# Performance work log

Measured on AMD Instinct MI355X. Metric: run time of the kernel, lower is better.

The kernel has to match this reference:

```python
import jax, jax.numpy as jnp
import numpy as np

N_NODES = 100000
N_EDGES = 3200000
N_GRAPHS = 256
VOCAB = 1500


def gcn_conv(x, edge_index, W, b, n_nodes):
    # x: [N, Fin], edge_index: [2, E] (row=source, col=target)
    h = x @ W  # [N, Fout]
    loops = jnp.arange(n_nodes, dtype=edge_index.dtype)
    row = jnp.concatenate([edge_index[0], loops])
    col = jnp.concatenate([edge_index[1], loops])
    # symmetric normalization with self-loops (PyG GCNConv default)
    deg = jax.ops.segment_sum(jnp.ones_like(col, dtype=h.dtype), col,
                              num_segments=n_nodes)
    dinv = jnp.where(deg > 0, jax.lax.rsqrt(deg), 0.0)
    norm = dinv[row] * dinv[col]  # [E+N]
    msg = h[row] * norm[:, None]  # gather + scale
    out = jax.ops.segment_sum(msg, col, num_segments=n_nodes)  # scatter-add
    return out + b


def setup_inputs() -> dict:
    key = jax.random.key(0)
    k = jax.random.split(key, 8)
    x_ids = jax.random.randint(k[0], (N_NODES,), 0, VOCAB)
    edge_index = jax.random.randint(k[1], (2, N_EDGES), 0, N_NODES)
    batch = jnp.sort(jax.random.randint(k[2], (N_NODES,), 0, N_GRAPHS))
    emb_table = jax.random.normal(k[3], (VOCAB, 16), dtype=jnp.float32)
    W1 = jax.random.normal(k[4], (16, 32), dtype=jnp.float32) * (1.0 / np.sqrt(16))
    b1 = jnp.zeros((32,), dtype=jnp.float32)
    W2 = jax.random.normal(k[5], (32, 41), dtype=jnp.float32) * (1.0 / np.sqrt(32))
    b2 = jnp.zeros((41,), dtype=jnp.float32)
    return {"x_ids": x_ids, "edge_index": edge_index, "batch": batch,
            "emb_table": emb_table, "W1": W1, "b1": b1, "W2": W2, "b2": b2}


def reference(x_ids, edge_index, batch, emb_table, W1, b1, W2, b2):
    x = emb_table[x_ids]                      # embedding lookup [N,16]
    x = gcn_conv(x, edge_index, W1, b1, N_NODES)
    x = jax.nn.relu(x)                        # dropout is identity in eval
    x = gcn_conv(x, edge_index, W2, b2, N_NODES)
    # scatter_add pooling over graphs in batch
    return jax.ops.segment_sum(x, batch, num_segments=N_GRAPHS)  # [G,41]
```

## Files before the change

### kernel.cpp

```cpp
#include <hip/hip_runtime.h>


constexpr int EPB = 16384;
constexpr int BSH = 8;
constexpr int BKTN = 1 << BSH;
constexpr int CAP = 10240;

__device__ inline unsigned short f2bf(float x) {
  unsigned u = __float_as_uint(x);
  u += 0x7FFF + ((u >> 16) & 1);
  return (unsigned short)(u >> 16);
}
__device__ inline float bf2f(unsigned short h) {
  return __uint_as_float((unsigned)h << 16);
}
__device__ inline unsigned pk(float a, float b) {
  return (unsigned)f2bf(a) | ((unsigned)f2bf(b) << 16);
}

__device__ __forceinline__ int swz(int b, int nblkp) {
  return (b & 7) * (nblkp >> 3) + (b >> 3);
}

__global__ __launch_bounds__(1024) void k_hist(const int* __restrict__ col, int E,
                                               int nbkt, int nblkp,
                                               int* __restrict__ hist) {
  __shared__ int h[512];
  int tid = threadIdx.x;
  int blk = swz(blockIdx.x, nblkp);
  for (int i = tid; i < nbkt; i += 1024) h[i] = 0;
  __syncthreads();
  int e0 = blk * EPB, e1 = min(E, e0 + EPB);
  for (int e = e0 + tid; e < e1; e += 1024) atomicAdd(&h[col[e] >> BSH], 1);
  __syncthreads();
  for (int b = tid; b < nbkt; b += 1024) hist[b * nblkp + blk] = h[b];
}

__global__ __launch_bounds__(1024) void k_scan_a(const int* __restrict__ hist, int tot,
                                                 int* __restrict__ off,
                                                 int* __restrict__ bsums) {
  __shared__ int sd[1024];
  int tid = threadIdx.x;
  int i = blockIdx.x * 1024 + tid;
  int v = (i < tot) ? hist[i] : 0;
  sd[tid] = v;
  __syncthreads();
  for (int o = 1; o < 1024; o <<= 1) {
    int u = (tid >= o) ? sd[tid - o] : 0;
    __syncthreads();
    sd[tid] += u;
    __syncthreads();
  }
  if (i < tot) off[i] = sd[tid] - v;
  if (tid == 1023) bsums[blockIdx.x] = sd[tid];
}

__global__ __launch_bounds__(1024) void k_scan_c(int tot, int nblkp, int nbkt, int E,
                                                 int nscan,
                                                 const int* __restrict__ bsums,
                                                 int* __restrict__ off,
                                                 int* __restrict__ bucket_off) {
  __shared__ int sd[1024];
  int tid = threadIdx.x, b = blockIdx.x;
  sd[tid] = (tid < b && tid < nscan) ? bsums[tid] : 0;
  __syncthreads();
  for (int o = 512; o >= 1; o >>= 1) {
    if (tid < o) sd[tid] += sd[tid + o];
    __syncthreads();
  }
  int sbase = sd[0];
  int i = b * 1024 + tid;
  if (i < tot) {
    int v = off[i] + sbase;
    off[i] = v;
    if (i % nblkp == 0) bucket_off[i / nblkp] = v;
  }
  if (i == 0) bucket_off[nbkt] = E;
}

__global__ __launch_bounds__(1024) void k_scatter(const int* __restrict__ row,
                                                  const int* __restrict__ col, int E,
                                                  int nbkt, int nblkp,
                                                  const int* __restrict__ off,
                                                  int* __restrict__ staging) {
  __shared__ int base[512];
  __shared__ int cur[512];
  int tid = threadIdx.x;
  int blk = swz(blockIdx.x, nblkp);
  for (int b = tid; b < nbkt; b += 1024) {
    base[b] = off[b * nblkp + blk];
    cur[b] = 0;
  }
  __syncthreads();
  int e0 = blk * EPB, e1 = min(E, e0 + EPB);
  for (int e = e0 + tid; e < e1; e += 1024) {
    int c = col[e];
    int b = c >> BSH;
    int rk = atomicAdd(&cur[b], 1);
    staging[base[b] + rk] = (row[e] << BSH) | (c & (BKTN - 1));
  }
}

__global__ __launch_bounds__(BKTN) void k_degprep(const int* __restrict__ staging,
                                                  const int* __restrict__ bucket_off,
                                                  const int* __restrict__ x_ids,
                                                  const float* __restrict__ emb,
                                                  int N,
                                                  float* __restrict__ dinv,
                                                  unsigned short* __restrict__ ag1) {
  __shared__ int cnt[BKTN];
  int tid = threadIdx.x, b = blockIdx.x;
  int beg = bucket_off[b], end = bucket_off[b + 1];
  cnt[tid] = 0;
  __syncthreads();
  for (int i = beg + tid; i < end; i += BKTN)
    atomicAdd(&cnt[staging[i] & (BKTN - 1)], 1);
  __syncthreads();
  int node = (b << BSH) + tid;
  if (node >= N) return;
  float d = rsqrtf((float)(cnt[tid] + 1));
  dinv[node] = d;
  const float* er = emb + (size_t)x_ids[node] * 16;
  float4 e0 = *(const float4*)(er);
  float4 e1 = *(const float4*)(er + 4);
  float4 e2 = *(const float4*)(er + 8);
  float4 e3 = *(const float4*)(er + 12);
  uint4 o0, o1;
  o0.x = pk(e0.x * d, e0.y * d); o0.y = pk(e0.z * d, e0.w * d);
  o0.z = pk(e1.x * d, e1.y * d); o0.w = pk(e1.z * d, e1.w * d);
  o1.x = pk(e2.x * d, e2.y * d); o1.y = pk(e2.z * d, e2.w * d);
  o1.z = pk(e3.x * d, e3.y * d); o1.w = pk(e3.z * d, e3.w * d);
  *(uint4*)(ag1 + (size_t)node * 16) = o0;
  *(uint4*)(ag1 + (size_t)node * 16 + 8) = o1;
}

__global__ __launch_bounds__(512) void k_fuse1(const unsigned short* __restrict__ ag1,
                                               const int* __restrict__ staging,
                                               const int* __restrict__ bucket_off,
                                               const float* __restrict__ dinv,
                                               const float* __restrict__ W1,
                                               const float* __restrict__ b1, int N,
                                               unsigned short* __restrict__ y1g) {
  __shared__ int list[CAP];
  __shared__ int cnt[BKTN], sc[BKTN], lcur[BKTN];
  __shared__ float W[512];
  __shared__ float bb[32];
  int tid = threadIdx.x, b = blockIdx.x;
  W[tid] = W1[tid];
  if (tid < 32) bb[tid] = b1[tid];
  int nloc = tid >> 1, half = tid & 1;
  int node = (b << BSH) + nloc;
  float acc[8];
  if (node < N) {
    uint4 v = *(const uint4*)(ag1 + (size_t)node * 16 + half * 8);
    acc[0] = bf2f(v.x & 0xFFFF); acc[1] = bf2f(v.x >> 16);
    acc[2] = bf2f(v.y & 0xFFFF); acc[3] = bf2f(v.y >> 16);
    acc[4] = bf2f(v.z & 0xFFFF); acc[5] = bf2f(v.z >> 16);
    acc[6] = bf2f(v.w & 0xFFFF); acc[7] = bf2f(v.w >> 16);
  } else {
#pragma unroll
    for (int k = 0; k < 8; ++k) acc[k] = 0.f;
  }
  int beg = bucket_off[b], end = bucket_off[b + 1];
  for (int cbeg = beg; cbeg < end; cbeg += CAP) {
    int cend = min(end, cbeg + CAP);
    if (tid < BKTN) cnt[tid] = 0;
    __syncthreads();
    for (int i = cbeg + tid; i < cend; i += 512)
      atomicAdd(&cnt[staging[i] & (BKTN - 1)], 1);
    __syncthreads();
    if (tid < BKTN) sc[tid] = cnt[tid];
    __syncthreads();
    for (int o = 1; o < BKTN; o <<= 1) {
      int u = (tid < BKTN && tid >= o) ? sc[tid - o] : 0;
      __syncthreads();
      if (tid < BKTN) sc[tid] += u;
      __syncthreads();
    }
    if (tid < BKTN) {
      int st = sc[tid] - cnt[tid];
      sc[tid] = st;
      lcur[tid] = st;
    }
    __syncthreads();
    for (int i = cbeg + tid; i < cend; i += 512) {
      int p = staging[i];
      int pos = atomicAdd(&lcur[p & (BKTN - 1)], 1);
      list[pos] = p >> BSH;
    }
    __syncthreads();
    if (node < N) {
      int st = sc[nloc], dg = cnt[nloc];
      for (int j = 0; j < dg; ++j) {
        int r = list[st + j];
        uint4 v = *(const uint4*)(ag1 + (size_t)r * 16 + half * 8);
        acc[0] += bf2f(v.x & 0xFFFF); acc[1] += bf2f(v.x >> 16);
        acc[2] += bf2f(v.y & 0xFFFF); acc[3] += bf2f(v.y >> 16);
        acc[4] += bf2f(v.z & 0xFFFF); acc[5] += bf2f(v.z >> 16);
        acc[6] += bf2f(v.w & 0xFFFF); acc[7] += bf2f(v.w >> 16);
      }
    }
    __syncthreads();
  }
  if (node >= N) return;
  float d = dinv[node];
  float sx[8], xo[8];
#pragma unroll
  for (int k = 0; k < 8; ++k) sx[k] = acc[k] * d;
#pragma unroll
  for (int k = 0; k < 8; ++k) xo[k] = __shfl_xor(sx[k], 1);
  float x[16];
  if (half == 0) {
#pragma unroll
    for (int k = 0; k < 8; ++k) { x[k] = sx[k]; x[8 + k] = xo[k]; }
  } else {
#pragma unroll
    for (int k = 0; k < 8; ++k) { x[k] = xo[k]; x[8 + k] = sx[k]; }
  }
  int j0 = half * 16;
  float a[16];
#pragma unroll
  for (int j = 0; j < 16; ++j) a[j] = bb[j0 + j];
#pragma unroll
  for (int k = 0; k < 16; ++k) {
    float xv = x[k];
#pragma unroll
    for (int j = 0; j < 16; ++j) a[j] += xv * W[k * 32 + j0 + j];
  }
#pragma unroll
  for (int j = 0; j < 16; ++j) a[j] = fmaxf(a[j], 0.f) * d;
  uint4 o0 = {pk(a[0], a[1]), pk(a[2], a[3]), pk(a[4], a[5]), pk(a[6], a[7])};
  uint4 o1 = {pk(a[8], a[9]), pk(a[10], a[11]), pk(a[12], a[13]), pk(a[14], a[15])};
  unsigned short* yp = y1g + (size_t)half * N * 16 + (size_t)node * 16;
  *(uint4*)(yp) = o0;
  *(uint4*)(yp + 8) = o1;
}

__global__ __launch_bounds__(512) void k_fuse2(const unsigned short* __restrict__ y1p,
                                               const int* __restrict__ staging,
                                               const int* __restrict__ bucket_off,
                                               const float* __restrict__ dinv,
                                               const int* __restrict__ batch, int N,
                                               int pofs, float* __restrict__ P) {
  __shared__ int list[CAP];
  __shared__ int cnt[BKTN], sc[BKTN], lcur[BKTN];
  __shared__ float pool[8 * 16];
  int tid = threadIdx.x, b = blockIdx.x;
  int nloc = tid >> 1, half = tid & 1;
  int node = (b << BSH) + nloc;
  float acc[8];
  if (node < N) {
    uint4 v = *(const uint4*)(y1p + (size_t)node * 16 + half * 8);
    acc[0] = bf2f(v.x & 0xFFFF); acc[1] = bf2f(v.x >> 16);
    acc[2] = bf2f(v.y & 0xFFFF); acc[3] = bf2f(v.y >> 16);
    acc[4] = bf2f(v.z & 0xFFFF); acc[5] = bf2f(v.z >> 16);
    acc[6] = bf2f(v.w & 0xFFFF); acc[7] = bf2f(v.w >> 16);
  } else {
#pragma unroll
    for (int k = 0; k < 8; ++k) acc[k] = 0.f;
  }
  int beg = bucket_off[b], end = bucket_off[b + 1];
  for (int cbeg = beg; cbeg < end; cbeg += CAP) {
    int cend = min(end, cbeg + CAP);
    if (tid < BKTN) cnt[tid] = 0;
    __syncthreads();
    for (int i = cbeg + tid; i < cend; i += 512)
      atomicAdd(&cnt[staging[i] & (BKTN - 1)], 1);
    __syncthreads();
    if (tid < BKTN) sc[tid] = cnt[tid];
    __syncthreads();
    for (int o = 1; o < BKTN; o <<= 1) {
      int u = (tid < BKTN && tid >= o) ? sc[tid - o] : 0;
      __syncthreads();
      if (tid < BKTN) sc[tid] += u;
      __syncthreads();
    }
    if (tid < BKTN) {
      int st = sc[tid] - cnt[tid];
      sc[tid] = st;
      lcur[tid] = st;
    }
    __syncthreads();
    for (int i = cbeg + tid; i < cend; i += 512) {
      int p = staging[i];
      int pos = atomicAdd(&lcur[p & (BKTN - 1)], 1);
      list[pos] = p >> BSH;
    }
    __syncthreads();
    if (node < N) {
      int st = sc[nloc], dg = cnt[nloc];
      for (int j = 0; j < dg; ++j) {
        int r = list[st + j];
        uint4 v = *(const uint4*)(y1p + (size_t)r * 16 + half * 8);
        acc[0] += bf2f(v.x & 0xFFFF); acc[1] += bf2f(v.x >> 16);
        acc[2] += bf2f(v.y & 0xFFFF); acc[3] += bf2f(v.y >> 16);
        acc[4] += bf2f(v.z & 0xFFFF); acc[5] += bf2f(v.z >> 16);
        acc[6] += bf2f(v.w & 0xFFFF); acc[7] += bf2f(v.w >> 16);
      }
    }
    __syncthreads();
  }
  int myg = -1;
  if (node < N) {
    float d = dinv[node];
#pragma unroll
    for (int k = 0; k < 8; ++k) acc[k] *= d;
    myg = batch[node];
  }
  int g0 = batch[b << BSH];
  int g1 = batch[min((b << BSH) + BKTN - 1, N - 1)];
  for (int clo = g0; clo <= g1; clo += 8) {
    for (int j = tid; j < 8 * 16; j += 512) pool[j] = 0.f;
    __syncthreads();
    if (myg >= clo && myg < clo + 8) {
      float* pp = pool + (myg - clo) * 16 + half * 8;
#pragma unroll
      for (int k = 0; k < 8; ++k) atomicAdd(pp + k, acc[k]);
    }
    __syncthreads();
    int ng = min(8, g1 - clo + 1);
    for (int j = tid; j < ng * 16; j += 512)
      atomicAdd(&P[(size_t)(clo + (j >> 4)) * 32 + pofs + (j & 15)], pool[j]);
    __syncthreads();
  }
}

__global__ __launch_bounds__(64) void k_final(const float* __restrict__ P,
                                              const int* __restrict__ batch, int N,
                                              const float* __restrict__ W2,
                                              const float* __restrict__ b2,
                                              float* __restrict__ out) {
  __shared__ float pr[32];
  __shared__ int se[2];
  int g = blockIdx.x, tid = threadIdx.x;
  if (tid < 2) {
    int v = g + tid;
    int lo = 0, hi = N;
    while (lo < hi) {
      int mid = (lo + hi) >> 1;
      if (batch[mid] < v) lo = mid + 1; else hi = mid;
    }
    se[tid] = lo;
  }
  if (tid < 32) pr[tid] = P[(size_t)g * 32 + tid];
  __syncthreads();
  if (tid < 41) {
    float o = (float)(se[1] - se[0]) * b2[tid];
#pragma unroll
    for (int k = 0; k < 32; ++k) o += pr[k] * W2[k * 41 + tid];
    out[(size_t)g * 41 + tid] = o;
  }
}

extern "C" void kernel_launch(void* const* d_in, const int* in_sizes, int n_in,
                              void* d_out, int out_size, void* d_ws, size_t ws_size,
                              hipStream_t stream) {
  const int* x_ids = (const int*)d_in[0];
  const int* edge_index = (const int*)d_in[1];
  const int* batch = (const int*)d_in[2];
  const float* emb = (const float*)d_in[3];
  const float* W1 = (const float*)d_in[4];
  const float* b1 = (const float*)d_in[5];
  const float* W2 = (const float*)d_in[6];
  const float* b2 = (const float*)d_in[7];
  float* out = (float*)d_out;

  const int N = in_sizes[0];
  const int E = in_sizes[1] / 2;
  const int G = out_size / 41;
  const int* row = edge_index;
  const int* col = edge_index + E;

  const int nbkt = (N + BKTN - 1) >> BSH;
  int nblk = (E + EPB - 1) / EPB;
  const int nblkp = (nblk + 7) & ~7;
  const int tot = nbkt * nblkp;
  const int nscan = (tot + 1023) >> 10;

  char* ws = (char*)d_ws;
  size_t woff = 0;
  auto alloc = [&](size_t bytes) -> char* {
    char* p = ws + woff;
    woff += (bytes + 255) & ~(size_t)255;
    return p;
  };
  int* staging = (int*)alloc((size_t)E * 4);
  float* dinv = (float*)alloc((size_t)N * 4);
  unsigned short* ag1 = (unsigned short*)alloc((size_t)N * 16 * 2);
  unsigned short* y1g = (unsigned short*)alloc((size_t)N * 32 * 2);
  int* hist = (int*)alloc((size_t)tot * 4);
  int* off = (int*)alloc((size_t)tot * 4);
  int* bucket_off = (int*)alloc(((size_t)nbkt + 1) * 4);
  int* bsums = (int*)alloc((size_t)nscan * 4);
  float* P = (float*)alloc((size_t)G * 32 * 4);
  (void)ws_size; (void)n_in;

  hipMemsetAsync(P, 0, (size_t)G * 32 * 4, stream);

  k_hist<<<nblkp, 1024, 0, stream>>>(col, E, nbkt, nblkp, hist);
  k_scan_a<<<nscan, 1024, 0, stream>>>(hist, tot, off, bsums);
  k_scan_c<<<nscan, 1024, 0, stream>>>(tot, nblkp, nbkt, E, nscan, bsums, off, bucket_off);
  k_scatter<<<nblkp, 1024, 0, stream>>>(row, col, E, nbkt, nblkp, off, staging);
  k_degprep<<<nbkt, BKTN, 0, stream>>>(staging, bucket_off, x_ids, emb, N, dinv, ag1);
  k_fuse1<<<nbkt, 512, 0, stream>>>(ag1, staging, bucket_off, dinv, W1, b1, N, y1g);
  k_fuse2<<<nbkt, 512, 0, stream>>>(y1g, staging, bucket_off, dinv, batch, N, 0, P);
  k_fuse2<<<nbkt, 512, 0, stream>>>(y1g + (size_t)N * 16, staging, bucket_off, dinv,
                                    batch, N, 16, P);
  k_final<<<G, 64, 0, stream>>>(P, batch, N, W2, b2, out);
}
```

Baseline: 236.6 us.

## Sort edges in LDS before scatter and unroll neighbor gathers by four

The scatter kernel now counts and prefix-sums bucket sizes locally, places each packed edge into a shared-memory buffer grouped by bucket, and then copies each bucket's run to global staging with one wave per bucket. Consecutive lanes now write consecutive global addresses, replacing the scattered per-edge global writes. Both aggregation kernels also unroll the neighbor gather loop four-wide so several independent row loads are in flight at once. The cost is a second read of col, a 64KB LDS buffer that limits occupancy, and extra barriers for the 512-entry scan.

```diff
diff --git a/kernel.cpp b/kernel.cpp
--- a/kernel.cpp
+++ b/kernel.cpp
@@ -16,6 +16,29 @@
 }
 __device__ inline unsigned pk(float a, float b) {
   return (unsigned)f2bf(a) | ((unsigned)f2bf(b) << 16);
+}
+__device__ __forceinline__ void add8(float acc[8], uint4 v) {
+  acc[0] += bf2f(v.x & 0xFFFF); acc[1] += bf2f(v.x >> 16);
+  acc[2] += bf2f(v.y & 0xFFFF); acc[3] += bf2f(v.y >> 16);
+  acc[4] += bf2f(v.z & 0xFFFF); acc[5] += bf2f(v.z >> 16);
+  acc[6] += bf2f(v.w & 0xFFFF); acc[7] += bf2f(v.w >> 16);
+}
+
+__device__ __forceinline__ void gather8(const unsigned short* __restrict__ base,
+                                        const int* list, int st, int dg,
+                                        float acc[8]) {
+  int j = 0;
+  for (; j + 4 <= dg; j += 4) {
+    int r0 = list[st + j], r1 = list[st + j + 1];
+    int r2 = list[st + j + 2], r3 = list[st + j + 3];
+    uint4 v0 = *(const uint4*)(base + (size_t)r0 * 16);
+    uint4 v1 = *(const uint4*)(base + (size_t)r1 * 16);
+    uint4 v2 = *(const uint4*)(base + (size_t)r2 * 16);
+    uint4 v3 = *(const uint4*)(base + (size_t)r3 * 16);
+    add8(acc, v0); add8(acc, v1); add8(acc, v2); add8(acc, v3);
+  }
+  for (; j < dg; ++j)
+    add8(acc, *(const uint4*)(base + (size_t)list[st + j] * 16));
 }
 
 __device__ __forceinline__ int swz(int b, int nblkp) {
@@ -83,21 +106,39 @@
                                                   int nbkt, int nblkp,
                                                   const int* __restrict__ off,
                                                   int* __restrict__ staging) {
-  __shared__ int base[512];
-  __shared__ int cur[512];
+  __shared__ int sbuf[EPB];
+  __shared__ int cnt[512], sc[512], cur[512];
   int tid = threadIdx.x;
+  int lane = tid & 63, wv = tid >> 6;
   int blk = swz(blockIdx.x, nblkp);
-  for (int b = tid; b < nbkt; b += 1024) {
-    base[b] = off[b * nblkp + blk];
-    cur[b] = 0;
-  }
+  if (tid < 512) cnt[tid] = 0;
   __syncthreads();
   int e0 = blk * EPB, e1 = min(E, e0 + EPB);
+  for (int e = e0 + tid; e < e1; e += 1024)
+    atomicAdd(&cnt[col[e] >> BSH], 1);
+  __syncthreads();
+  if (tid < 512) sc[tid] = cnt[tid];
+  __syncthreads();
+  for (int o = 1; o < 512; o <<= 1) {
+    int u = (tid < 512 && tid >= o) ? sc[tid - o] : 0;
+    __syncthreads();
+    if (tid < 512) sc[tid] += u;
+    __syncthreads();
+  }
+  if (tid < 512) { int st = sc[tid] - cnt[tid]; sc[tid] = st; cur[tid] = st; }
+  __syncthreads();
   for (int e = e0 + tid; e < e1; e += 1024) {
     int c = col[e];
     int b = c >> BSH;
-    int rk = atomicAdd(&cur[b], 1);
-    staging[base[b] + rk] = (row[e] << BSH) | (c & (BKTN - 1));
+    int pos = atomicAdd(&cur[b], 1);
+    sbuf[pos] = (row[e] << BSH) | (c & (BKTN - 1));
+  }
+  __syncthreads();
+  for (int b = wv; b < nbkt; b += 16) {
+    int lbeg = sc[b], lcnt = cnt[b];
+    int g = off[b * nblkp + blk];
+    for (int j = lane; j < lcnt; j += 64)
+      staging[g + j] = sbuf[lbeg + j];
   }
 }
 
@@ -189,17 +230,7 @@
       list[pos] = p >> BSH;
     }
     __syncthreads();
-    if (node < N) {
-      int st = sc[nloc], dg = cnt[nloc];
-      for (int j = 0; j < dg; ++j) {
-        int r = list[st + j];
-        uint4 v = *(const uint4*)(ag1 + (size_t)r * 16 + half * 8);
-        acc[0] += bf2f(v.x & 0xFFFF); acc[1] += bf2f(v.x >> 16);
-        acc[2] += bf2f(v.y & 0xFFFF); acc[3] += bf2f(v.y >> 16);
-        acc[4] += bf2f(v.z & 0xFFFF); acc[5] += bf2f(v.z >> 16);
-        acc[6] += bf2f(v.w & 0xFFFF); acc[7] += bf2f(v.w >> 16);
-      }
-    }
+    if (node < N) gather8(ag1 + half * 8, list, sc[nloc], cnt[nloc], acc);
     __syncthreads();
   }
   if (node >= N) return;
@@ -287,17 +318,7 @@
       list[pos] = p >> BSH;
     }
     __syncthreads();
-    if (node < N) {
-      int st = sc[nloc], dg = cnt[nloc];
-      for (int j = 0; j < dg; ++j) {
-        int r = list[st + j];
-        uint4 v = *(const uint4*)(y1p + (size_t)r * 16 + half * 8);
-        acc[0] += bf2f(v.x & 0xFFFF); acc[1] += bf2f(v.x >> 16);
-        acc[2] += bf2f(v.y & 0xFFFF); acc[3] += bf2f(v.y >> 16);
-        acc[4] += bf2f(v.z & 0xFFFF); acc[5] += bf2f(v.z >> 16);
-        acc[6] += bf2f(v.w & 0xFFFF); acc[7] += bf2f(v.w >> 16);
-      }
-    }
+    if (node < N) gather8(y1p + half * 8, list, sc[nloc], cnt[nloc], acc);
     __syncthreads();
   }
   int myg = -1;
```

New measurement: 239.5 us. About the same (+1.2%).
